# Kernel tuning notes

Measured on AMD Instinct MI355X. Metric: run time of the kernel, lower is better.

The kernel has to match this reference:

```python
import jax, jax.numpy as jnp
import numpy as np

N_QUBITS = 4
N_LAYERS = 3
BATCH = 1048576  # 2**20; batched state vector [B, 2,2,2,2] complex64 = 128 MB


def setup_inputs() -> dict:
    key = jax.random.key(0)
    k1, k2 = jax.random.split(key)
    x = jax.random.normal(k1, (BATCH, N_QUBITS), dtype=jnp.float32)
    q_weights = jax.random.normal(k2, (N_LAYERS, N_QUBITS, 3), dtype=jnp.float32) * 0.1
    return {"x": x, "q_weights": q_weights}


def _ry_mat(theta):
    # RY(t) = [[cos t/2, -sin t/2], [sin t/2, cos t/2]]; theta: [] or [B]
    c = jnp.cos(theta * 0.5).astype(jnp.complex64)
    s = jnp.sin(theta * 0.5).astype(jnp.complex64)
    return jnp.stack([jnp.stack([c, -s], -1), jnp.stack([s, c], -1)], -2)


def _rz_mat(theta):
    # RZ(t) = diag(e^{-it/2}, e^{it/2})
    e = jnp.exp(-0.5j * theta.astype(jnp.complex64))
    z = jnp.zeros_like(e)
    return jnp.stack([jnp.stack([e, z], -1), jnp.stack([z, jnp.conj(e)], -1)], -2)


def _apply_1q(state, U, wire):
    # state: [B,2,2,2,2]; U: [2,2] (shared) or [B,2,2] (per-sample)
    ax = wire + 1
    state = jnp.moveaxis(state, ax, -1)
    if U.ndim == 3:
        state = jnp.einsum('b...o,bno->b...n', state, U)
    else:
        state = jnp.einsum('b...o,no->b...n', state, U)
    return jnp.moveaxis(state, -1, ax)


def _cnot(state, c, t):
    # flip target bit on the control=1 slice
    ca, ta = c + 1, t + 1
    s0 = jnp.take(state, 0, axis=ca)
    s1 = jnp.take(state, 1, axis=ca)
    ta2 = ta if ta < ca else ta - 1
    s1 = jnp.flip(s1, axis=ta2)
    return jnp.stack([s0, s1], axis=ca)


def _circuit(x, q_weights):
    B = x.shape[0]
    xn = jnp.tanh(x) * jnp.pi  # [B, 4]
    # |0000>
    state = jnp.zeros((B,) + (2,) * N_QUBITS, dtype=jnp.complex64)
    state = state.at[:, 0, 0, 0, 0].set(1.0 + 0.0j)
    # angle encoding: RY(2x_i) then RZ(x_i), per-sample batched 2x2 gates
    for i in range(N_QUBITS):
        state = _apply_1q(state, _ry_mat(2.0 * xn[:, i]), i)
        state = _apply_1q(state, _rz_mat(xn[:, i]), i)
    # variational layers: Rot(phi,theta,omega) = RZ(omega) @ RY(theta) @ RZ(phi)
    for l in range(N_LAYERS):
        for i in range(N_QUBITS):
            phi, theta, omega = q_weights[l, i, 0], q_weights[l, i, 1], q_weights[l, i, 2]
            U = _rz_mat(omega) @ _ry_mat(theta) @ _rz_mat(phi)
            state = _apply_1q(state, U, i)
        for i in range(N_QUBITS):
            state = _cnot(state, i, (i + 1) % N_QUBITS)
    # <Z_i> = p(bit_i=0) - p(bit_i=1)
    probs = jnp.abs(state) ** 2  # [B,2,2,2,2] real
    evs = []
    for i in range(N_QUBITS):
        axes = tuple(a for a in range(1, N_QUBITS + 1) if a != i + 1)
        marg = jnp.sum(probs, axis=axes)  # [B, 2]
        evs.append(marg[:, 0] - marg[:, 1])
    return jnp.stack(evs, axis=-1).astype(jnp.float32)  # [B, 4]


def reference(x, q_weights):
    return _circuit(x, q_weights)
```

## Files before the change

### kernel.cpp

```cpp
#include <hip/hip_runtime.h>

#define PI_F 3.14159265358979323846f

__device__ __forceinline__ float2 cmul(float2 a, float2 b) {
    return make_float2(fmaf(a.x, b.x, -(a.y * b.y)), fmaf(a.x, b.y, a.y * b.x));
}
__device__ __forceinline__ float2 cadd(float2 a, float2 b) {
    return make_float2(a.x + b.x, a.y + b.y);
}

__device__ __forceinline__ float tanh_fast(float x) {
    float ax = fabsf(x);
    float e = __expf(-2.0f * ax);
    float t = (1.0f - e) / (1.0f + e);
    return copysignf(t, x);
}

template <int BP>
__device__ __forceinline__ void apply_gate(float2 st[16], float2 u00, float2 u01,
                                           float2 u10, float2 u11) {
#pragma unroll
    for (int i = 0; i < 8; i++) {
        const int lo = ((i >> BP) << (BP + 1)) | (i & ((1 << BP) - 1));
        const int hi = lo | (1 << BP);
        float2 a = st[lo], b = st[hi];
        st[lo] = cadd(cmul(u00, a), cmul(u01, b));
        st[hi] = cadd(cmul(u10, a), cmul(u11, b));
    }
}

template <int CB, int TB>
__device__ __forceinline__ void cnot(float2 st[16]) {
#pragma unroll
    for (int i = 0; i < 16; i++) {
        if ((i & (1 << CB)) && !(i & (1 << TB))) {
            float2 t = st[i];
            st[i] = st[i | (1 << TB)];
            st[i | (1 << TB)] = t;
        }
    }
}

__global__ __launch_bounds__(256) void qlayer_kernel(const float* __restrict__ x,
                                                     const float* __restrict__ qw,
                                                     float* __restrict__ out, int B) {
    __shared__ float2 Ug[12][4];
    const int tid = threadIdx.x;
    if (tid < 12) {
        const float phi = qw[tid * 3 + 0];
        const float th  = qw[tid * 3 + 1];
        const float om  = qw[tid * 3 + 2];
        float s, c;   __sincosf(0.5f * th, &s, &c);
        float sa, ca; __sincosf(0.5f * (phi + om), &sa, &ca);
        float sb, cb; __sincosf(0.5f * (phi - om), &sb, &cb);
        Ug[tid][0] = make_float2(c * ca, -c * sa);
        Ug[tid][1] = make_float2(-s * cb, -s * sb);
        Ug[tid][2] = make_float2(s * cb, -s * sb);
        Ug[tid][3] = make_float2(c * ca, c * sa);
    }
    __syncthreads();

    const int b = blockIdx.x * 256 + tid;
    if (b >= B) return;

    const float4 xv = reinterpret_cast<const float4*>(x)[b];
    const float xs[4] = {xv.x, xv.y, xv.z, xv.w};

    float2 v[4][2];
#pragma unroll
    for (int q = 0; q < 4; q++) {
        const float xn = tanh_fast(xs[q]) * PI_F;
        float s, c;   __sincosf(xn, &s, &c);
        float sh, ch; __sincosf(0.5f * xn, &sh, &ch);
        v[q][0] = make_float2(c * ch, -c * sh);
        v[q][1] = make_float2(s * ch, s * sh);
    }

#pragma unroll
    for (int q = 0; q < 4; q++) {
        const float2 u00 = Ug[q][0], u01 = Ug[q][1], u10 = Ug[q][2], u11 = Ug[q][3];
        const float2 a = v[q][0], bb = v[q][1];
        v[q][0] = cadd(cmul(u00, a), cmul(u01, bb));
        v[q][1] = cadd(cmul(u10, a), cmul(u11, bb));
    }

    float2 st[16];
#pragma unroll
    for (int i = 0; i < 16; i++) {
        const float2 t01 = cmul(v[0][(i >> 3) & 1], v[1][(i >> 2) & 1]);
        const float2 t23 = cmul(v[2][(i >> 1) & 1], v[3][i & 1]);
        st[i] = cmul(t01, t23);
    }

    cnot<3, 2>(st); cnot<2, 1>(st); cnot<1, 0>(st); cnot<0, 3>(st);

#pragma unroll
    for (int l = 1; l < 3; l++) {
        apply_gate<3>(st, Ug[l * 4 + 0][0], Ug[l * 4 + 0][1], Ug[l * 4 + 0][2], Ug[l * 4 + 0][3]);
        apply_gate<2>(st, Ug[l * 4 + 1][0], Ug[l * 4 + 1][1], Ug[l * 4 + 1][2], Ug[l * 4 + 1][3]);
        apply_gate<1>(st, Ug[l * 4 + 2][0], Ug[l * 4 + 2][1], Ug[l * 4 + 2][2], Ug[l * 4 + 2][3]);
        apply_gate<0>(st, Ug[l * 4 + 3][0], Ug[l * 4 + 3][1], Ug[l * 4 + 3][2], Ug[l * 4 + 3][3]);
        cnot<3, 2>(st); cnot<2, 1>(st); cnot<1, 0>(st); cnot<0, 3>(st);
    }

    float p[16];
#pragma unroll
    for (int i = 0; i < 16; i++) p[i] = fmaf(st[i].x, st[i].x, st[i].y * st[i].y);

    float4 ev = make_float4(0.f, 0.f, 0.f, 0.f);
#pragma unroll
    for (int i = 0; i < 16; i++) {
        ev.x += (i & 8) ? -p[i] : p[i];
        ev.y += (i & 4) ? -p[i] : p[i];
        ev.z += (i & 2) ? -p[i] : p[i];
        ev.w += (i & 1) ? -p[i] : p[i];
    }
    reinterpret_cast<float4*>(out)[b] = ev;
}

extern "C" void kernel_launch(void* const* d_in, const int* in_sizes, int n_in,
                              void* d_out, int out_size, void* d_ws, size_t ws_size,
                              hipStream_t stream) {
    const float* x  = (const float*)d_in[0];
    const float* qw = (const float*)d_in[1];
    float* out = (float*)d_out;
    const int B = in_sizes[0] / 4;
    const int blocks = (B + 255) / 256;
    qlayer_kernel<<<blocks, 256, 0, stream>>>(x, qw, out, B);
}
```

Baseline: 98.77 us.

## Cut ALU work with hardware transcendentals, fused complex FMAs and normalization-based expectations

Replaces the tanh/sincos path with raw hardware exp2/rcp/sin/cos builtins and derives the full-angle sin and cos from the half-angle ones by double-angle identities. Gate application now uses a fused complex multiply-add chain, and the gate matrices are packed as float4 in LDS so each is read in fewer loads. The initial product state reuses pairwise products instead of recomputing them, and the expectation values use the unit norm, computing 1 - 2*p(bit=1) with fewer additions. The intent is to shrink the per-thread instruction count in what may be an ALU-bound kernel. It risks small accuracy differences from the approximate builtins and from assuming the state norm is exactly one.

```diff
diff --git a/kernel.cpp b/kernel.cpp
--- a/kernel.cpp
+++ b/kernel.cpp
@@ -2,18 +2,13 @@
 
 #define PI_F 3.14159265358979323846f
 
+__device__ __forceinline__ float2 cmadd2(float2 u, float2 a, float2 w, float2 b) {
+    float re = fmaf(u.x, a.x, fmaf(-u.y, a.y, fmaf(w.x, b.x, -(w.y * b.y))));
+    float im = fmaf(u.x, a.y, fmaf(u.y, a.x, fmaf(w.x, b.y, w.y * b.x)));
+    return make_float2(re, im);
+}
 __device__ __forceinline__ float2 cmul(float2 a, float2 b) {
     return make_float2(fmaf(a.x, b.x, -(a.y * b.y)), fmaf(a.x, b.y, a.y * b.x));
-}
-__device__ __forceinline__ float2 cadd(float2 a, float2 b) {
-    return make_float2(a.x + b.x, a.y + b.y);
-}
-
-__device__ __forceinline__ float tanh_fast(float x) {
-    float ax = fabsf(x);
-    float e = __expf(-2.0f * ax);
-    float t = (1.0f - e) / (1.0f + e);
-    return copysignf(t, x);
 }
 
 template <int BP>
@@ -24,8 +19,8 @@
         const int lo = ((i >> BP) << (BP + 1)) | (i & ((1 << BP) - 1));
         const int hi = lo | (1 << BP);
         float2 a = st[lo], b = st[hi];
-        st[lo] = cadd(cmul(u00, a), cmul(u01, b));
-        st[hi] = cadd(cmul(u10, a), cmul(u11, b));
+        st[lo] = cmadd2(u00, a, u01, b);
+        st[hi] = cmadd2(u10, a, u11, b);
     }
 }
 
@@ -44,7 +39,7 @@
 __global__ __launch_bounds__(256) void qlayer_kernel(const float* __restrict__ x,
                                                      const float* __restrict__ qw,
                                                      float* __restrict__ out, int B) {
-    __shared__ float2 Ug[12][4];
+    __shared__ float4 Ug[12][2];
     const int tid = threadIdx.x;
     if (tid < 12) {
         const float phi = qw[tid * 3 + 0];
@@ -53,10 +48,8 @@
         float s, c;   __sincosf(0.5f * th, &s, &c);
         float sa, ca; __sincosf(0.5f * (phi + om), &sa, &ca);
         float sb, cb; __sincosf(0.5f * (phi - om), &sb, &cb);
-        Ug[tid][0] = make_float2(c * ca, -c * sa);
-        Ug[tid][1] = make_float2(-s * cb, -s * sb);
-        Ug[tid][2] = make_float2(s * cb, -s * sb);
-        Ug[tid][3] = make_float2(c * ca, c * sa);
+        Ug[tid][0] = make_float4(c * ca, -c * sa, -s * cb, -s * sb);
+        Ug[tid][1] = make_float4(s * cb, -s * sb, c * ca, c * sa);
     }
     __syncthreads();
 
@@ -69,37 +62,56 @@
     float2 v[4][2];
 #pragma unroll
     for (int q = 0; q < 4; q++) {
-        const float xn = tanh_fast(xs[q]) * PI_F;
-        float s, c;   __sincosf(xn, &s, &c);
-        float sh, ch; __sincosf(0.5f * xn, &sh, &ch);
-        v[q][0] = make_float2(c * ch, -c * sh);
+        const float xq = xs[q];
+        const float ax = fabsf(xq);
+        const float e  = __builtin_amdgcn_exp2f(ax * -2.8853900817779268f);
+        const float r  = __builtin_amdgcn_rcpf(1.0f + e);
+        const float t  = copysignf((1.0f - e) * r, xq);
+        const float sh = __builtin_amdgcn_sinf(t * 0.25f);
+        const float ch = __builtin_amdgcn_cosf(t * 0.25f);
+        const float s  = 2.0f * sh * ch;
+        const float c  = fmaf(-2.0f * sh, sh, 1.0f);
+        v[q][0] = make_float2(c * ch, -(c * sh));
         v[q][1] = make_float2(s * ch, s * sh);
     }
 
 #pragma unroll
     for (int q = 0; q < 4; q++) {
-        const float2 u00 = Ug[q][0], u01 = Ug[q][1], u10 = Ug[q][2], u11 = Ug[q][3];
+        const float4 A = Ug[q][0], Bq = Ug[q][1];
+        const float2 u00 = make_float2(A.x, A.y),  u01 = make_float2(A.z, A.w);
+        const float2 u10 = make_float2(Bq.x, Bq.y), u11 = make_float2(Bq.z, Bq.w);
         const float2 a = v[q][0], bb = v[q][1];
-        v[q][0] = cadd(cmul(u00, a), cmul(u01, bb));
-        v[q][1] = cadd(cmul(u10, a), cmul(u11, bb));
+        v[q][0] = cmadd2(u00, a, u01, bb);
+        v[q][1] = cmadd2(u10, a, u11, bb);
     }
 
+    float2 t01[4], t23[4];
+#pragma unroll
+    for (int i = 0; i < 4; i++) {
+        t01[i] = cmul(v[0][(i >> 1) & 1], v[1][i & 1]);
+        t23[i] = cmul(v[2][(i >> 1) & 1], v[3][i & 1]);
+    }
     float2 st[16];
 #pragma unroll
-    for (int i = 0; i < 16; i++) {
-        const float2 t01 = cmul(v[0][(i >> 3) & 1], v[1][(i >> 2) & 1]);
-        const float2 t23 = cmul(v[2][(i >> 1) & 1], v[3][i & 1]);
-        st[i] = cmul(t01, t23);
-    }
+    for (int i = 0; i < 16; i++) st[i] = cmul(t01[i >> 2], t23[i & 3]);
 
     cnot<3, 2>(st); cnot<2, 1>(st); cnot<1, 0>(st); cnot<0, 3>(st);
 
 #pragma unroll
     for (int l = 1; l < 3; l++) {
-        apply_gate<3>(st, Ug[l * 4 + 0][0], Ug[l * 4 + 0][1], Ug[l * 4 + 0][2], Ug[l * 4 + 0][3]);
-        apply_gate<2>(st, Ug[l * 4 + 1][0], Ug[l * 4 + 1][1], Ug[l * 4 + 1][2], Ug[l * 4 + 1][3]);
-        apply_gate<1>(st, Ug[l * 4 + 2][0], Ug[l * 4 + 2][1], Ug[l * 4 + 2][2], Ug[l * 4 + 2][3]);
-        apply_gate<0>(st, Ug[l * 4 + 3][0], Ug[l * 4 + 3][1], Ug[l * 4 + 3][2], Ug[l * 4 + 3][3]);
+#pragma unroll
+        for (int q = 0; q < 4; q++) {
+            const int g = l * 4 + q;
+            const float4 A = Ug[g][0], Bq = Ug[g][1];
+            const float2 u00 = make_float2(A.x, A.y),  u01 = make_float2(A.z, A.w);
+            const float2 u10 = make_float2(Bq.x, Bq.y), u11 = make_float2(Bq.z, Bq.w);
+            switch (q) {
+                case 0: apply_gate<3>(st, u00, u01, u10, u11); break;
+                case 1: apply_gate<2>(st, u00, u01, u10, u11); break;
+                case 2: apply_gate<1>(st, u00, u01, u10, u11); break;
+                case 3: apply_gate<0>(st, u00, u01, u10, u11); break;
+            }
+        }
         cnot<3, 2>(st); cnot<2, 1>(st); cnot<1, 0>(st); cnot<0, 3>(st);
     }
 
@@ -107,14 +119,21 @@
 #pragma unroll
     for (int i = 0; i < 16; i++) p[i] = fmaf(st[i].x, st[i].x, st[i].y * st[i].y);
 
-    float4 ev = make_float4(0.f, 0.f, 0.f, 0.f);
+    float pr[8];
 #pragma unroll
-    for (int i = 0; i < 16; i++) {
-        ev.x += (i & 8) ? -p[i] : p[i];
-        ev.y += (i & 4) ? -p[i] : p[i];
-        ev.z += (i & 2) ? -p[i] : p[i];
-        ev.w += (i & 1) ? -p[i] : p[i];
-    }
+    for (int j = 0; j < 8; j++) pr[j] = p[2 * j] + p[2 * j + 1];
+
+    const float s3 = (pr[4] + pr[5]) + (pr[6] + pr[7]);
+    const float s2 = (pr[2] + pr[3]) + (pr[6] + pr[7]);
+    const float s1 = (pr[1] + pr[3]) + (pr[5] + pr[7]);
+    const float s0 = ((p[1] + p[3]) + (p[5] + p[7])) +
+                     ((p[9] + p[11]) + (p[13] + p[15]));
+
+    float4 ev;
+    ev.x = fmaf(-2.0f, s3, 1.0f);
+    ev.y = fmaf(-2.0f, s2, 1.0f);
+    ev.z = fmaf(-2.0f, s1, 1.0f);
+    ev.w = fmaf(-2.0f, s0, 1.0f);
     reinterpret_cast<float4*>(out)[b] = ev;
 }
 
```

New measurement: 96.65 us. -2.1%, faster.
